# Kernel tuning notes

Hardware: AMD Instinct MI355X
Metric: run time of the kernel (lower is better)

The kernel has to match this reference:

```python
import jax, jax.numpy as jnp
import numpy as np

EPS = 1e-5
TAU_MAX = 1.0  # undefined global in source; assumed 1.0


def _conv4d(x, w, b, stride):
    # x: [N,C,T,X,Y,Z], w: [O,I,kt,kx,ky,kz], VALID padding (dense equivalent of strided Minkowski conv)
    dn = jax.lax.conv_dimension_numbers(x.shape, w.shape, ('NCTXYZ', 'OITXYZ', 'NCTXYZ'))
    y = jax.lax.conv_general_dilated(x, w, window_strides=stride, padding='VALID', dimension_numbers=dn)
    return y + b.reshape(1, -1, 1, 1, 1, 1)


def _bn(x, g, b, m, v):
    # inference-mode batchnorm over channel axis 1
    shape = (1, -1) + (1,) * (x.ndim - 2)
    return (x - m.reshape(shape)) * (g.reshape(shape) / jnp.sqrt(v.reshape(shape) + EPS)) + b.reshape(shape)


def setup_inputs() -> dict:
    key = jax.random.key(0)
    ks = jax.random.split(key, 32)
    f32 = jnp.float32
    d = {}
    d['x'] = jax.random.normal(ks[0], (4, 2, 6, 120, 120, 96), f32)
    d['jnt_pos'] = jax.random.normal(ks[1], (4, 6), f32)
    d['jnt_goal'] = jax.random.normal(ks[2], (4, 6), f32)
    # conv1: 2->64, k3 s3
    d['w1'] = jax.random.normal(ks[3], (64, 2, 3, 3, 3, 3), f32) * 0.05
    d['b1'] = jax.random.normal(ks[4], (64,), f32) * 0.05
    d['g1'] = jax.random.uniform(ks[5], (64,), f32, 0.5, 1.5)
    d['be1'] = jax.random.normal(ks[6], (64,), f32) * 0.05
    d['m1'] = jax.random.normal(ks[7], (64,), f32) * 0.05
    d['v1'] = jax.random.uniform(ks[8], (64,), f32, 0.5, 1.5)
    # conv2: 64->128, k2 s2
    d['w2'] = jax.random.normal(ks[9], (128, 64, 2, 2, 2, 2), f32) * 0.05
    d['b2'] = jax.random.normal(ks[10], (128,), f32) * 0.05
    d['g2'] = jax.random.uniform(ks[11], (128,), f32, 0.5, 1.5)
    d['be2'] = jax.random.normal(ks[12], (128,), f32) * 0.05
    d['m2'] = jax.random.normal(ks[13], (128,), f32) * 0.05
    d['v2'] = jax.random.uniform(ks[14], (128,), f32, 0.5, 1.5)
    # conv4: 128->256, k=(1,10,10,8) s=(1,10,10,8)
    d['w4'] = jax.random.normal(ks[15], (256, 128, 1, 10, 10, 8), f32) * 0.02
    d['b4'] = jax.random.normal(ks[16], (256,), f32) * 0.05
    # norm (BatchNorm1d(256))
    d['gn'] = jax.random.uniform(ks[17], (256,), f32, 0.5, 1.5)
    d['ben'] = jax.random.normal(ks[18], (256,), f32) * 0.05
    d['mn'] = jax.random.normal(ks[19], (256,), f32) * 0.05
    d['vn'] = jax.random.uniform(ks[20], (256,), f32, 0.5, 1.5)
    # linear: 256+12 -> 512, + BN
    d['wl'] = jax.random.normal(ks[21], (512, 268), f32) * 0.05
    d['bl'] = jax.random.normal(ks[22], (512,), f32) * 0.05
    d['gl'] = jax.random.uniform(ks[23], (512,), f32, 0.5, 1.5)
    d['bel'] = jax.random.normal(ks[24], (512,), f32) * 0.05
    d['ml'] = jax.random.normal(ks[25], (512,), f32) * 0.05
    d['vl'] = jax.random.uniform(ks[26], (512,), f32, 0.5, 1.5)
    # out: 512 -> 6
    d['wo'] = jax.random.normal(ks[27], (6, 512), f32) * 0.05
    d['bo'] = jax.random.normal(ks[28], (6,), f32) * 0.05
    return d


def reference(x, jnt_pos, jnt_goal, w1, b1, g1, be1, m1, v1, w2, b2, g2, be2, m2, v2,
              w4, b4, gn, ben, mn, vn, wl, bl, gl, bel, ml, vl, wo, bo):
    # pool1: max pool (1,2,2,2) stride (1,2,2,2)
    h = jax.lax.reduce_window(x, -jnp.inf, jax.lax.max,
                              window_dimensions=(1, 1, 1, 2, 2, 2),
                              window_strides=(1, 1, 1, 2, 2, 2), padding='VALID')
    h = jax.nn.relu(_bn(_conv4d(h, w1, b1, (3, 3, 3, 3)), g1, be1, m1, v1))
    h = jax.nn.relu(_bn(_conv4d(h, w2, b2, (2, 2, 2, 2)), g2, be2, m2, v2))
    h = _conv4d(h, w4, b4, (1, 10, 10, 8))          # [B,256,1,1,1,1]
    h = jnp.max(h, axis=(2, 3, 4, 5))               # global max pool -> [B,256]
    # to_dense_tnsr is an identity scatter (row b <- row b) after global pooling
    h = jax.nn.relu(_bn(h, gn, ben, mn, vn))
    # dropout eval-mode = identity
    h = jnp.concatenate([jnt_pos, jnt_goal, h], axis=1)   # [B,268]
    h = jax.nn.relu(_bn(h @ wl.T + bl, gl, bel, ml, vl))  # [B,512]
    return jnp.tanh(h @ wo.T + bo) * TAU_MAX              # [B,6]
```

## Files before the change

### kernel.cpp

```cpp
#include <hip/hip_runtime.h>
#include <hip/hip_bf16.h>


typedef float f32x4_t __attribute__((ext_vector_type(4)));

__device__ __forceinline__ float wave_reduce(float v) {
#pragma unroll
    for (int off = 32; off > 0; off >>= 1) v += __shfl_down(v, off);
    return v;
}

__global__ __launch_bounds__(256) void k_prep(
    const float* __restrict__ w1, const float* __restrict__ w2,
    float* __restrict__ w1t, float* __restrict__ w2t) {
    int tid = threadIdx.x;
    if (blockIdx.x < 64) {
        __shared__ float tile[32][65];
        int oc = blockIdx.x >> 4;
        int tc = blockIdx.x & 15;
        int o0 = oc * 32, t0 = tc * 64;
        int ol = tid >> 6, tl = tid & 63;
#pragma unroll
        for (int p = 0; p < 8; ++p) {
            int o = ol + p * 4;
            tile[o][tl] = w2[(size_t)(o0 + o) * 1024 + t0 + tl];
        }
        __syncthreads();
        int ow = tid & 31, tw = tid >> 5;
#pragma unroll
        for (int p = 0; p < 8; ++p) {
            int t = tw + p * 8;
            w2t[(size_t)(t0 + t) * 128 + o0 + ow] = tile[ow][t];
        }
        return;
    }
    for (int i = (blockIdx.x - 64) * 256 + tid; i < 64 * 162; i += 16 * 256) {
        int t = i >> 6, o = i & 63;
        w1t[i] = w1[o * 162 + t];
    }
}

__global__ __launch_bounds__(256) void k_conv1(
    const float* __restrict__ x, const float* __restrict__ w1t,
    const float* __restrict__ b1, const float* __restrict__ g1,
    const float* __restrict__ be1, const float* __restrict__ m1,
    const float* __restrict__ v1, float* __restrict__ y1) {
    int bid = blockIdx.x;
    int yo = bid % 20; bid /= 20;
    int xo = bid % 20; bid /= 20;
    int t  = bid % 2;  bid /= 2;
    int n  = bid;

    __shared__ float pooled[2592];
    int tid = threadIdx.x;

    for (int task = tid; task < 1296; task += 256) {
        int q = task % 24; int r = task / 24;
        int py = r % 3; r /= 3;
        int px = r % 3; r /= 3;
        int tp = r % 3; int c = r / 3;
        const float* base = x + ((((size_t)n * 2 + c) * 6 + 3 * t + tp) * 120 + 6 * xo + 2 * px) * 11520
                              + (size_t)(6 * yo + 2 * py) * 96 + 4 * q;
        float4 v00 = *(const float4*)(base);
        float4 v01 = *(const float4*)(base + 96);
        float4 v10 = *(const float4*)(base + 11520);
        float4 v11 = *(const float4*)(base + 11520 + 96);
        float p0 = fmaxf(fmaxf(fmaxf(v00.x, v00.y), fmaxf(v01.x, v01.y)),
                         fmaxf(fmaxf(v10.x, v10.y), fmaxf(v11.x, v11.y)));
        float p1 = fmaxf(fmaxf(fmaxf(v00.z, v00.w), fmaxf(v01.z, v01.w)),
                         fmaxf(fmaxf(v10.z, v10.w), fmaxf(v11.z, v11.w)));
        int row = ((c * 3 + tp) * 3 + px) * 3 + py;
        int z0 = 2 * q, z1 = 2 * q + 1;
        pooled[row * 48 + (z0 % 3) * 16 + z0 / 3] = p0;
        pooled[row * 48 + (z1 % 3) * 16 + z1 / 3] = p1;
    }
    __syncthreads();

    int o  = tid & 63;
    int zg = tid >> 6;
    float acc[4] = {0.f, 0.f, 0.f, 0.f};
    for (int row = 0; row < 54; ++row) {
        const float* pr = &pooled[row * 48 + zg * 4];
#pragma unroll
        for (int kz = 0; kz < 3; ++kz) {
            float w = w1t[(row * 3 + kz) * 64 + o];
            float4 pv = *(const float4*)(pr + kz * 16);
            acc[0] = fmaf(w, pv.x, acc[0]);
            acc[1] = fmaf(w, pv.y, acc[1]);
            acc[2] = fmaf(w, pv.z, acc[2]);
            acc[3] = fmaf(w, pv.w, acc[3]);
        }
    }
    float s  = g1[o] * rsqrtf(v1[o] + 1e-5f);
    float sh = be1[o] + (b1[o] - m1[o]) * s;
    size_t obase = ((((size_t)n * 64 + o) * 2 + t) * 20 + xo) * 320 + (size_t)yo * 16 + zg * 4;
    float4 outv;
    outv.x = fmaxf(acc[0] * s + sh, 0.f);
    outv.y = fmaxf(acc[1] * s + sh, 0.f);
    outv.z = fmaxf(acc[2] * s + sh, 0.f);
    outv.w = fmaxf(acc[3] * s + sh, 0.f);
    *(float4*)&y1[obase] = outv;
}

__global__ __launch_bounds__(512) void k_conv2(
    const float* __restrict__ y1, const float* __restrict__ w2t,
    const float* __restrict__ b2, const float* __restrict__ g2,
    const float* __restrict__ be2, const float* __restrict__ m2,
    const float* __restrict__ v2, float* __restrict__ y2) {
    int bid = blockIdx.x;
    int yo = bid % 10; bid /= 10;
    int xo = bid % 10; bid /= 10;
    int n  = bid;

    __shared__ float in2t[8192];
    __shared__ float red[8192];
    int tid = threadIdx.x;
#pragma unroll
    for (int it = 0; it < 4; ++it) {
        int task = tid + it * 512;
        int a = task & 3; int row = task >> 2;
        int ky = row & 1, kx = (row >> 1) & 1, kt = (row >> 2) & 1, c = row >> 3;
        const float* src = y1 + ((((size_t)n * 64 + c) * 2 + kt) * 20 + 2 * xo + kx) * 320
                              + (size_t)(2 * yo + ky) * 16 + 4 * a;
        float4 v = *(const float4*)src;
        *(float2*)&in2t[row * 8 + 2 * a]        = make_float2(v.x, v.z);
        *(float2*)&in2t[4096 + row * 8 + 2 * a] = make_float2(v.y, v.w);
    }
    __syncthreads();

    int o2 = tid & 63;
    int ks = tid >> 6;
    float acc[2][8];
#pragma unroll
    for (int a = 0; a < 2; ++a)
#pragma unroll
        for (int b = 0; b < 8; ++b) acc[a][b] = 0.f;

    for (int rr = 0; rr < 64; ++rr) {
        int row = ks * 64 + rr;
#pragma unroll
        for (int kz = 0; kz < 2; ++kz) {
            float2 w = *(const float2*)&w2t[(row * 2 + kz) * 128 + 2 * o2];
            float4 p0 = *(const float4*)&in2t[kz * 4096 + row * 8];
            float4 p1 = *(const float4*)&in2t[kz * 4096 + row * 8 + 4];
            acc[0][0] = fmaf(w.x, p0.x, acc[0][0]);
            acc[0][1] = fmaf(w.x, p0.y, acc[0][1]);
            acc[0][2] = fmaf(w.x, p0.z, acc[0][2]);
            acc[0][3] = fmaf(w.x, p0.w, acc[0][3]);
            acc[0][4] = fmaf(w.x, p1.x, acc[0][4]);
            acc[0][5] = fmaf(w.x, p1.y, acc[0][5]);
            acc[0][6] = fmaf(w.x, p1.z, acc[0][6]);
            acc[0][7] = fmaf(w.x, p1.w, acc[0][7]);
            acc[1][0] = fmaf(w.y, p0.x, acc[1][0]);
            acc[1][1] = fmaf(w.y, p0.y, acc[1][1]);
            acc[1][2] = fmaf(w.y, p0.z, acc[1][2]);
            acc[1][3] = fmaf(w.y, p0.w, acc[1][3]);
            acc[1][4] = fmaf(w.y, p1.x, acc[1][4]);
            acc[1][5] = fmaf(w.y, p1.y, acc[1][5]);
            acc[1][6] = fmaf(w.y, p1.z, acc[1][6]);
            acc[1][7] = fmaf(w.y, p1.w, acc[1][7]);
        }
    }
#pragma unroll
    for (int a = 0; a < 2; ++a)
#pragma unroll
        for (int b = 0; b < 8; ++b) red[ks * 1024 + o2 * 16 + a * 8 + b] = acc[a][b];
    __syncthreads();

#pragma unroll
    for (int e = tid; e < 1024; e += 512) {
        float v = 0.f;
#pragma unroll
        for (int k = 0; k < 8; ++k) v += red[k * 1024 + e];
        int o2e = e >> 4, i = e & 15;
        int o = o2e * 2 + (i >> 3), zo = i & 7;
        float s  = g2[o] * rsqrtf(v2[o] + 1e-5f);
        float sh = be2[o] + (b2[o] - m2[o]) * s;
        y2[(((size_t)n * 128 + o) * 10 + xo) * 80 + (size_t)yo * 8 + zo] = fmaxf(v * s + sh, 0.f);
    }
}

__global__ __launch_bounds__(256) void k_conv4(
    const float* __restrict__ y2, const float* __restrict__ w4,
    float* __restrict__ part) {
    int oc = blockIdx.x & 63;
    int kc = blockIdx.x >> 6;
    int tid = threadIdx.x;
    const float4* y2v = (const float4*)y2;
    const f32x4_t* w4v = (const f32x4_t*)w4;
    float acc[4][4];
#pragma unroll
    for (int a = 0; a < 4; ++a)
#pragma unroll
        for (int b = 0; b < 4; ++b) acc[a][b] = 0.f;

    int base = kc * 2560;
#pragma unroll 2
    for (int i = 0; i < 10; ++i) {
        int f4 = base + i * 256 + tid;
        float4 a0 = y2v[f4];
        float4 a1 = y2v[25600 + f4];
        float4 a2 = y2v[51200 + f4];
        float4 a3 = y2v[76800 + f4];
#pragma unroll
        for (int oo = 0; oo < 4; ++oo) {
            f32x4_t w = __builtin_nontemporal_load(&w4v[(size_t)(oc * 4 + oo) * 25600 + f4]);
            acc[oo][0] = fmaf(w.x, a0.x, fmaf(w.y, a0.y, fmaf(w.z, a0.z, fmaf(w.w, a0.w, acc[oo][0]))));
            acc[oo][1] = fmaf(w.x, a1.x, fmaf(w.y, a1.y, fmaf(w.z, a1.z, fmaf(w.w, a1.w, acc[oo][1]))));
            acc[oo][2] = fmaf(w.x, a2.x, fmaf(w.y, a2.y, fmaf(w.z, a2.z, fmaf(w.w, a2.w, acc[oo][2]))));
            acc[oo][3] = fmaf(w.x, a3.x, fmaf(w.y, a3.y, fmaf(w.z, a3.z, fmaf(w.w, a3.w, acc[oo][3]))));
        }
    }
    __shared__ float red[4][16];
    int wave = tid >> 6, lane = tid & 63;
#pragma unroll
    for (int oo = 0; oo < 4; ++oo)
#pragma unroll
        for (int nn = 0; nn < 4; ++nn) {
            float v = wave_reduce(acc[oo][nn]);
            if (lane == 0) red[wave][oo * 4 + nn] = v;
        }
    __syncthreads();
    if (tid < 16) {
        float sum = red[0][tid] + red[1][tid] + red[2][tid] + red[3][tid];
        part[(size_t)blockIdx.x * 16 + tid] = sum;
    }
}

__global__ __launch_bounds__(256) void k_lin1(
    const float* __restrict__ part, const float* __restrict__ b4,
    const float* __restrict__ gn, const float* __restrict__ ben,
    const float* __restrict__ mn, const float* __restrict__ vn,
    const float* __restrict__ jp, const float* __restrict__ jg,
    const float* __restrict__ wl, const float* __restrict__ bl,
    const float* __restrict__ gl, const float* __restrict__ bel,
    const float* __restrict__ ml, const float* __restrict__ vl,
    float* __restrict__ h2) {
    __shared__ float feat[4 * 268];
    int tid = threadIdx.x;
    {
        int o = tid;
        int oc = o >> 2, oo = o & 3;
        float s  = gn[o] * rsqrtf(vn[o] + 1e-5f);
        float sh = ben[o] + (b4[o] - mn[o]) * s;
#pragma unroll
        for (int nn = 0; nn < 4; ++nn) {
            float acc = 0.f;
#pragma unroll
            for (int kc = 0; kc < 10; ++kc) acc += part[(kc * 64 + oc) * 16 + oo * 4 + nn];
            feat[nn * 268 + 12 + o] = fmaxf(acc * s + sh, 0.f);
        }
        if (o < 24) {
            int nn = o / 6, j = o % 6;
            feat[nn * 268 + j] = jp[o];
            feat[nn * 268 + 6 + j] = jg[o];
        }
    }
    __syncthreads();

    int wave = tid >> 6, lane = tid & 63;
    int j = blockIdx.x * 4 + wave;
    const float* wr = wl + (size_t)j * 268;
    float acc[4] = {0.f, 0.f, 0.f, 0.f};
    for (int k = lane; k < 268; k += 64) {
        float w = wr[k];
#pragma unroll
        for (int nn = 0; nn < 4; ++nn) acc[nn] = fmaf(w, feat[nn * 268 + k], acc[nn]);
    }
#pragma unroll
    for (int nn = 0; nn < 4; ++nn) acc[nn] = wave_reduce(acc[nn]);
    if (lane == 0) {
        float s  = gl[j] * rsqrtf(vl[j] + 1e-5f);
        float sh = bel[j] + (bl[j] - ml[j]) * s;
#pragma unroll
        for (int nn = 0; nn < 4; ++nn) h2[nn * 512 + j] = fmaxf(acc[nn] * s + sh, 0.f);
    }
}

__global__ void k_lin2(const float* __restrict__ h2, const float* __restrict__ wo,
                       const float* __restrict__ bo, float* __restrict__ out) {
    int wave = threadIdx.x >> 6, lane = threadIdx.x & 63;
    int n = wave;
    float hv[8];
#pragma unroll
    for (int i = 0; i < 8; ++i) hv[i] = h2[n * 512 + i * 64 + lane];
    for (int o = 0; o < 6; ++o) {
        float acc = 0.f;
#pragma unroll
        for (int i = 0; i < 8; ++i) acc = fmaf(hv[i], wo[o * 512 + i * 64 + lane], acc);
        acc = wave_reduce(acc);
        if (lane == 0) out[n * 6 + o] = tanhf(acc + bo[o]);
    }
}

extern "C" void kernel_launch(void* const* d_in, const int* in_sizes, int n_in,
                              void* d_out, int out_size, void* d_ws, size_t ws_size,
                              hipStream_t stream) {
    const float* x   = (const float*)d_in[0];
    const float* jp  = (const float*)d_in[1];
    const float* jg  = (const float*)d_in[2];
    const float* w1  = (const float*)d_in[3];
    const float* b1  = (const float*)d_in[4];
    const float* g1  = (const float*)d_in[5];
    const float* be1 = (const float*)d_in[6];
    const float* m1  = (const float*)d_in[7];
    const float* v1  = (const float*)d_in[8];
    const float* w2  = (const float*)d_in[9];
    const float* b2  = (const float*)d_in[10];
    const float* g2  = (const float*)d_in[11];
    const float* be2 = (const float*)d_in[12];
    const float* m2  = (const float*)d_in[13];
    const float* v2  = (const float*)d_in[14];
    const float* w4  = (const float*)d_in[15];
    const float* b4  = (const float*)d_in[16];
    const float* gn  = (const float*)d_in[17];
    const float* ben = (const float*)d_in[18];
    const float* mn  = (const float*)d_in[19];
    const float* vn  = (const float*)d_in[20];
    const float* wl  = (const float*)d_in[21];
    const float* bl  = (const float*)d_in[22];
    const float* gl  = (const float*)d_in[23];
    const float* bel = (const float*)d_in[24];
    const float* ml  = (const float*)d_in[25];
    const float* vl  = (const float*)d_in[26];
    const float* wo  = (const float*)d_in[27];
    const float* bo  = (const float*)d_in[28];
    float* out = (float*)d_out;

    float* ws   = (float*)d_ws;
    float* w1t  = ws;
    float* w2t  = ws + 10368;
    float* y1   = ws + 141440;
    float* y2   = ws + 3418240;
    float* part = ws + 3827840;
    float* h2   = ws + 3838080;

    k_prep<<<80, 256, 0, stream>>>(w1, w2, w1t, w2t);
    k_conv1<<<3200, 256, 0, stream>>>(x, w1t, b1, g1, be1, m1, v1, y1);
    k_conv2<<<400, 512, 0, stream>>>(y1, w2t, b2, g2, be2, m2, v2, y2);
    k_conv4<<<640, 256, 0, stream>>>(y2, w4, part);
    k_lin1<<<128, 256, 0, stream>>>(part, b4, gn, ben, mn, vn, jp, jg,
                                    wl, bl, gl, bel, ml, vl, h2);
    k_lin2<<<1, 256, 0, stream>>>(h2, wo, bo, out);
}
```

Before: 122.6 us.

## Software-pipeline conv1: prefetch next tile's input into registers during compute

Each conv1 block now handles two adjacent y-output tiles and double-buffers the pooled shared tile. While the first tile's FMA loop runs, the global loads for the second tile are already in flight in registers, with a sched_barrier keeping the loads ahead of the compute. The aim is to hide global-load latency that the single-tile kernel exposed before compute started. In exchange, register pressure rises (96 floats of prefetch per thread, launch_bounds min 2 blocks), shared memory doubles, and the grid is halved, which lowers parallelism.

```diff
diff --git a/kernel.cpp b/kernel.cpp
--- a/kernel.cpp
+++ b/kernel.cpp
@@ -40,47 +40,61 @@
     }
 }
 
-__global__ __launch_bounds__(256) void k_conv1(
-    const float* __restrict__ x, const float* __restrict__ w1t,
+__device__ __forceinline__ void c1_issue(
+    const float* __restrict__ x, int n, int t, int xo, int yo, int tid,
+    float4 rg[6][4]) {
+#pragma unroll
+    for (int it = 0; it < 6; ++it) {
+        if (it < 5 || tid < 16) {
+            int task = tid + it * 256;
+            int q = task % 24; int r = task / 24;
+            int py = r % 3; r /= 3;
+            int px = r % 3; r /= 3;
+            int tp = r % 3; int c = r / 3;
+            const float* base = x + ((((size_t)n * 2 + c) * 6 + 3 * t + tp) * 120 + 6 * xo + 2 * px) * 11520
+                                  + (size_t)(6 * yo + 2 * py) * 96 + 4 * q;
+            rg[it][0] = *(const float4*)(base);
+            rg[it][1] = *(const float4*)(base + 96);
+            rg[it][2] = *(const float4*)(base + 11520);
+            rg[it][3] = *(const float4*)(base + 11520 + 96);
+        }
+    }
+}
+
+__device__ __forceinline__ void c1_commit(int tid, const float4 rg[6][4],
+                                          float* __restrict__ pbuf) {
+#pragma unroll
+    for (int it = 0; it < 6; ++it) {
+        if (it < 5 || tid < 16) {
+            int task = tid + it * 256;
+            int q = task % 24; int r = task / 24;
+            int py = r % 3; r /= 3;
+            int px = r % 3; r /= 3;
+            int tp = r % 3; int c = r / 3;
+            float4 v00 = rg[it][0], v01 = rg[it][1], v10 = rg[it][2], v11 = rg[it][3];
+            float p0 = fmaxf(fmaxf(fmaxf(v00.x, v00.y), fmaxf(v01.x, v01.y)),
+                             fmaxf(fmaxf(v10.x, v10.y), fmaxf(v11.x, v11.y)));
+            float p1 = fmaxf(fmaxf(fmaxf(v00.z, v00.w), fmaxf(v01.z, v01.w)),
+                             fmaxf(fmaxf(v10.z, v10.w), fmaxf(v11.z, v11.w)));
+            int row = ((c * 3 + tp) * 3 + px) * 3 + py;
+            int z0 = 2 * q, z1 = 2 * q + 1;
+            pbuf[row * 48 + (z0 % 3) * 16 + z0 / 3] = p0;
+            pbuf[row * 48 + (z1 % 3) * 16 + z1 / 3] = p1;
+        }
+    }
+}
+
+__device__ __forceinline__ void c1_compute(
+    const float* __restrict__ pbuf, const float* __restrict__ w1t,
     const float* __restrict__ b1, const float* __restrict__ g1,
     const float* __restrict__ be1, const float* __restrict__ m1,
-    const float* __restrict__ v1, float* __restrict__ y1) {
-    int bid = blockIdx.x;
-    int yo = bid % 20; bid /= 20;
-    int xo = bid % 20; bid /= 20;
-    int t  = bid % 2;  bid /= 2;
-    int n  = bid;
-
-    __shared__ float pooled[2592];
-    int tid = threadIdx.x;
-
-    for (int task = tid; task < 1296; task += 256) {
-        int q = task % 24; int r = task / 24;
-        int py = r % 3; r /= 3;
-        int px = r % 3; r /= 3;
-        int tp = r % 3; int c = r / 3;
-        const float* base = x + ((((size_t)n * 2 + c) * 6 + 3 * t + tp) * 120 + 6 * xo + 2 * px) * 11520
-                              + (size_t)(6 * yo + 2 * py) * 96 + 4 * q;
-        float4 v00 = *(const float4*)(base);
-        float4 v01 = *(const float4*)(base + 96);
-        float4 v10 = *(const float4*)(base + 11520);
-        float4 v11 = *(const float4*)(base + 11520 + 96);
-        float p0 = fmaxf(fmaxf(fmaxf(v00.x, v00.y), fmaxf(v01.x, v01.y)),
-                         fmaxf(fmaxf(v10.x, v10.y), fmaxf(v11.x, v11.y)));
-        float p1 = fmaxf(fmaxf(fmaxf(v00.z, v00.w), fmaxf(v01.z, v01.w)),
-                         fmaxf(fmaxf(v10.z, v10.w), fmaxf(v11.z, v11.w)));
-        int row = ((c * 3 + tp) * 3 + px) * 3 + py;
-        int z0 = 2 * q, z1 = 2 * q + 1;
-        pooled[row * 48 + (z0 % 3) * 16 + z0 / 3] = p0;
-        pooled[row * 48 + (z1 % 3) * 16 + z1 / 3] = p1;
-    }
-    __syncthreads();
-
+    const float* __restrict__ v1, float* __restrict__ y1,
+    int n, int t, int xo, int yo, int tid) {
     int o  = tid & 63;
     int zg = tid >> 6;
     float acc[4] = {0.f, 0.f, 0.f, 0.f};
     for (int row = 0; row < 54; ++row) {
-        const float* pr = &pooled[row * 48 + zg * 4];
+        const float* pr = pbuf + row * 48 + zg * 4;
 #pragma unroll
         for (int kz = 0; kz < 3; ++kz) {
             float w = w1t[(row * 3 + kz) * 64 + o];
@@ -100,6 +114,32 @@
     outv.z = fmaxf(acc[2] * s + sh, 0.f);
     outv.w = fmaxf(acc[3] * s + sh, 0.f);
     *(float4*)&y1[obase] = outv;
+}
+
+__global__ __launch_bounds__(256, 2) void k_conv1(
+    const float* __restrict__ x, const float* __restrict__ w1t,
+    const float* __restrict__ b1, const float* __restrict__ g1,
+    const float* __restrict__ be1, const float* __restrict__ m1,
+    const float* __restrict__ v1, float* __restrict__ y1) {
+    int bid = blockIdx.x;
+    int yp = bid % 10; bid /= 10;
+    int xo = bid % 20; bid /= 20;
+    int t  = bid % 2;
+    int n  = bid / 2;
+    int tid = threadIdx.x;
+
+    __shared__ float pooled[2][2592];
+    float4 rg[6][4];
+
+    c1_issue(x, n, t, xo, 2 * yp, tid, rg);
+    c1_commit(tid, rg, pooled[0]);
+    __syncthreads();
+    c1_issue(x, n, t, xo, 2 * yp + 1, tid, rg);
+    __builtin_amdgcn_sched_barrier(0);
+    c1_compute(pooled[0], w1t, b1, g1, be1, m1, v1, y1, n, t, xo, 2 * yp, tid);
+    c1_commit(tid, rg, pooled[1]);
+    __syncthreads();
+    c1_compute(pooled[1], w1t, b1, g1, be1, m1, v1, y1, n, t, xo, 2 * yp + 1, tid);
 }
 
 __global__ __launch_bounds__(512) void k_conv2(
@@ -336,7 +376,7 @@
     float* h2   = ws + 3838080;
 
     k_prep<<<80, 256, 0, stream>>>(w1, w2, w1t, w2t);
-    k_conv1<<<3200, 256, 0, stream>>>(x, w1t, b1, g1, be1, m1, v1, y1);
+    k_conv1<<<1600, 256, 0, stream>>>(x, w1t, b1, g1, be1, m1, v1, y1);
     k_conv2<<<400, 512, 0, stream>>>(y1, w2t, b2, g2, be2, m2, v2, y2);
     k_conv4<<<640, 256, 0, stream>>>(y2, w4, part);
     k_lin1<<<128, 256, 0, stream>>>(part, b4, gn, ben, mn, vn, jp, jg,
```

Result: slower. 141.5 us (+15.4%).

## Split max-pool into a separate kernel with fully coalesced loads before conv1

Applied to the files above, without the earlier changes.

Max pooling moves out of conv1 into a dedicated kernel that streams contiguous input slabs through shared memory and writes a pooled tensor to workspace. Conv1 then reads the 8x smaller pooled tensor with simple contiguous float4 loads instead of strided 4-point gathers. The aim is better coalescing on the large input read, at the cost of an extra kernel launch and a round trip of the pooled tensor (about 33 MB) through global memory.

```diff
diff --git a/kernel.cpp b/kernel.cpp
--- a/kernel.cpp
+++ b/kernel.cpp
@@ -40,8 +40,34 @@
     }
 }
 
+__global__ __launch_bounds__(256) void k_pool(
+    const float* __restrict__ x, float* __restrict__ xp) {
+    int b = blockIdx.x;
+    int xq = b % 60; int r = b / 60;
+    int tr = r % 6;  r /= 6;
+    int c  = r % 2;  int n = r / 2;
+    int tid = threadIdx.x;
+
+    __shared__ float zbuf[11520];
+
+    const float4* slab = (const float4*)(x + ((((size_t)n * 2 + c) * 6 + tr) * 120 + 2 * xq) * 11520);
+    for (int f = tid; f < 5760; f += 256) {
+        float4 v = slab[f];
+        int xi = f / 2880, rem = f - xi * 2880;
+        *(float2*)&zbuf[xi * 5760 + rem * 2] = make_float2(fmaxf(v.x, v.y), fmaxf(v.z, v.w));
+    }
+    __syncthreads();
+    float* outb = xp + (size_t)b * 2880;
+    for (int o = tid; o < 2880; o += 256) {
+        int yp = o / 48, zp = o - yp * 48;
+        const float* z0 = &zbuf[2 * yp * 48 + zp];
+        float m = fmaxf(fmaxf(z0[0], z0[48]), fmaxf(z0[5760], z0[5760 + 48]));
+        outb[o] = m;
+    }
+}
+
 __global__ __launch_bounds__(256) void k_conv1(
-    const float* __restrict__ x, const float* __restrict__ w1t,
+    const float* __restrict__ xp, const float* __restrict__ w1t,
     const float* __restrict__ b1, const float* __restrict__ g1,
     const float* __restrict__ be1, const float* __restrict__ m1,
     const float* __restrict__ v1, float* __restrict__ y1) {
@@ -50,29 +76,25 @@
     int xo = bid % 20; bid /= 20;
     int t  = bid % 2;  bid /= 2;
     int n  = bid;
+    int tid = threadIdx.x;
 
     __shared__ float pooled[2592];
-    int tid = threadIdx.x;
-
-    for (int task = tid; task < 1296; task += 256) {
-        int q = task % 24; int r = task / 24;
-        int py = r % 3; r /= 3;
-        int px = r % 3; r /= 3;
-        int tp = r % 3; int c = r / 3;
-        const float* base = x + ((((size_t)n * 2 + c) * 6 + 3 * t + tp) * 120 + 6 * xo + 2 * px) * 11520
-                              + (size_t)(6 * yo + 2 * py) * 96 + 4 * q;
-        float4 v00 = *(const float4*)(base);
-        float4 v01 = *(const float4*)(base + 96);
-        float4 v10 = *(const float4*)(base + 11520);
-        float4 v11 = *(const float4*)(base + 11520 + 96);
-        float p0 = fmaxf(fmaxf(fmaxf(v00.x, v00.y), fmaxf(v01.x, v01.y)),
-                         fmaxf(fmaxf(v10.x, v10.y), fmaxf(v11.x, v11.y)));
-        float p1 = fmaxf(fmaxf(fmaxf(v00.z, v00.w), fmaxf(v01.z, v01.w)),
-                         fmaxf(fmaxf(v10.z, v10.w), fmaxf(v11.z, v11.w)));
+
+    for (int task = tid; task < 648; task += 256) {
+        int seg = task / 36, rem = task - seg * 36;
+        int c = seg / 9, tp = (seg % 9) / 3, px = seg % 3;
+        const float* src = xp + ((((size_t)n * 2 + c) * 6 + 3 * t + tp) * 60 + 3 * xo + px) * 2880
+                              + (size_t)(3 * yo) * 48 + rem * 4;
+        float4 v = *(const float4*)src;
+        int zz = rem * 4;
+        int py = zz / 48, zq = zz - py * 48;
         int row = ((c * 3 + tp) * 3 + px) * 3 + py;
-        int z0 = 2 * q, z1 = 2 * q + 1;
-        pooled[row * 48 + (z0 % 3) * 16 + z0 / 3] = p0;
-        pooled[row * 48 + (z1 % 3) * 16 + z1 / 3] = p1;
+        float vs[4] = {v.x, v.y, v.z, v.w};
+#pragma unroll
+        for (int j = 0; j < 4; ++j) {
+            int z = zq + j;
+            pooled[row * 48 + (z % 3) * 16 + z / 3] = vs[j];
+        }
     }
     __syncthreads();
 
@@ -334,9 +356,11 @@
     float* y2   = ws + 3418240;
     float* part = ws + 3827840;
     float* h2   = ws + 3838080;
+    float* xp   = ws + 3840128;
 
     k_prep<<<80, 256, 0, stream>>>(w1, w2, w1t, w2t);
-    k_conv1<<<3200, 256, 0, stream>>>(x, w1t, b1, g1, be1, m1, v1, y1);
+    k_pool<<<2880, 256, 0, stream>>>(x, xp);
+    k_conv1<<<3200, 256, 0, stream>>>(xp, w1t, b1, g1, be1, m1, v1, y1);
     k_conv2<<<400, 512, 0, stream>>>(y1, w2t, b2, g2, be2, m2, v2, y2);
     k_conv4<<<640, 256, 0, stream>>>(y2, w4, part);
     k_lin1<<<128, 256, 0, stream>>>(part, b4, gn, ben, mn, vn, jp, jg,
```

Result: slower. 161.6 us (+31.8%).
